# Kernel tuning notes

Hardware: AMD Instinct MI355X
Metric: run time of the kernel (lower is better)

Reference implementation:

```python
import jax, jax.numpy as jnp
import numpy as np

WCD, WCOV, WQUAL = 1.0, 1e-4, 1e-4
BIG = 1e10  # penalty to exclude zero-rows from min/argmin


def _calus(x, y):
    # x: [B, N, 3], y: [B, M, 3]
    B, N, _ = x.shape
    M = y.shape[1]
    # _remove_zero_rows filters rows whose coordinate SUM is zero -> mask instead
    mx = x.sum(-1) != 0  # [B, N] valid x points
    my = y.sum(-1) != 0  # [B, M] valid y points
    dt = x.dtype
    # squared pairwise distances d[b, j, i] = ||x[b,i] - y[b,j]||^2  (expanded form)
    xn = jnp.sum(x * x, axis=-1)  # [B, N]
    yn = jnp.sum(y * y, axis=-1)  # [B, M]
    d = yn[:, :, None] + xn[:, None, :] - 2.0 * jnp.einsum('bmc,bnc->bmn', y, x)  # [B, M, N]
    # push invalid rows/cols out of every min
    d = d + jnp.where(mx, 0.0, BIG).astype(dt)[:, None, :] \
          + jnp.where(my, 0.0, BIG).astype(dt)[:, :, None]
    x_min = jnp.min(d, axis=1)     # [B, N] nearest-y distance per x point
    x_arg = jnp.argmin(d, axis=1)  # [B, N] index into y
    y_min = jnp.min(d, axis=2)     # [B, M] nearest-x distance per y point
    y_arg = jnp.argmin(d, axis=2)  # [B, M] index into x
    fmx, fmy = mx.astype(dt), my.astype(dt)
    nx, ny = fmx.sum(-1), fmy.sum(-1)  # valid counts per sample
    # chamfer = mean over x-points + mean over y-points (torch cat+sum)
    cd = jnp.sum(x_min * fmx, -1) / nx + jnp.sum(y_min * fmy, -1) / ny  # [B]
    # coverage: fraction of y indices hit by some valid x point (unique count)
    rows = jnp.arange(B)[:, None]
    hit_y = jnp.zeros((B, M), dt).at[rows, x_arg].max(fmx)
    cov = hit_y.sum(-1) / ny  # [B]
    # quality: fraction of x indices hit by some valid y point
    hit_x = jnp.zeros((B, N), dt).at[rows, y_arg].max(fmy)
    qual = hit_x.sum(-1) / nx  # [B]
    return cd.mean(), cov.mean(), qual.mean()


def setup_inputs() -> dict:
    key = jax.random.key(0)
    kx, ky = jax.random.split(key)
    B, N, M = 32, 2048, 2048
    x = jax.random.normal(kx, (B, N, 3), dtype=jnp.float32)
    y = jax.random.normal(ky, (B, M, 3), dtype=jnp.float32)
    return {"x": x, "y": y}


def reference(x, y):
    cd, cov, qual = _calus(x, y)
    val = WCD * cd - WCOV * cov - WQUAL * qual
    return (val, cd, cov, qual)
```

## Files before the change

### kernel.cpp

```cpp
#include <hip/hip_runtime.h>
#include <stdint.h>


#define BB 32
#define NP 2048
#define NPTS (BB * NP)
#define BIGF 1e10f

typedef unsigned int u32;

__global__ __launch_bounds__(256) void pack_kernel(const float* __restrict__ x,
                                                   const float* __restrict__ y,
                                                   float4* __restrict__ pk) {
  int t = blockIdx.x * 256 + threadIdx.x;
  int side = t >> 16;
  int i = t & (NPTS - 1);
  const float* src = side ? y : x;
  float v0 = src[3 * i], v1 = src[3 * i + 1], v2 = src[3 * i + 2];
  float vn = v0 * v0 + v1 * v1 + v2 * v2;
  if (v0 + v1 + v2 == 0.0f) vn += BIGF;
  pk[t] = make_float4(v0, v1, v2, vn);
}

#define EMB(d, jg) __uint_as_float((__float_as_uint(d) & 0xFFFFF800u) | (u32)(jg))

__global__ __launch_bounds__(512) void nn_kernel(const float4* __restrict__ pk,
                                                 u32* __restrict__ hitpart,
                                                 float* __restrict__ sums_part,
                                                 float* __restrict__ cnts_part) {
  int bid = blockIdx.x;
  int side = bid >> 8;
  int b = (bid >> 3) & 31;
  int pc = bid & 7;
  int tid = threadIdx.x;
  int w = __builtin_amdgcn_readfirstlane(tid >> 6);
  int lane = tid & 63;

  __shared__ u32 merged[8][256];
  __shared__ float pws[256];
  __shared__ u32 hitlds[64];
  __shared__ float redc[8], redn[8];

  const float4* pbase = pk + side * NPTS + b * NP + pc * 256;
  float pmx[4], pmy[4], pmz[4];
  for (int k = 0; k < 4; ++k) {
    float4 p = pbase[lane + 64 * k];
    pmx[k] = -2.0f * p.x; pmy[k] = -2.0f * p.y; pmz[k] = -2.0f * p.z;
    if (w == 0) pws[lane + 64 * k] = p.w;
  }
  if (tid < 64) hitlds[tid] = 0u;

  const float4* qq = pk + (side ^ 1) * NPTS + b * NP + w * 256;
  u32 qoff = (u32)(w * 256);
  float best0 = 3.0e38f, best1 = 3.0e38f, best2 = 3.0e38f, best3 = 3.0e38f;

#define PROC2(qA, qB, jg)                                                          \
  {                                                                                \
    float a0 = fmaf((qA).x, pmx[0], fmaf((qA).y, pmy[0], fmaf((qA).z, pmz[0], (qA).w))); \
    float a1 = fmaf((qA).x, pmx[1], fmaf((qA).y, pmy[1], fmaf((qA).z, pmz[1], (qA).w))); \
    float a2 = fmaf((qA).x, pmx[2], fmaf((qA).y, pmy[2], fmaf((qA).z, pmz[2], (qA).w))); \
    float a3 = fmaf((qA).x, pmx[3], fmaf((qA).y, pmy[3], fmaf((qA).z, pmz[3], (qA).w))); \
    float b0 = fmaf((qB).x, pmx[0], fmaf((qB).y, pmy[0], fmaf((qB).z, pmz[0], (qB).w))); \
    float b1 = fmaf((qB).x, pmx[1], fmaf((qB).y, pmy[1], fmaf((qB).z, pmz[1], (qB).w))); \
    float b2 = fmaf((qB).x, pmx[2], fmaf((qB).y, pmy[2], fmaf((qB).z, pmz[2], (qB).w))); \
    float b3 = fmaf((qB).x, pmx[3], fmaf((qB).y, pmy[3], fmaf((qB).z, pmz[3], (qB).w))); \
    best0 = fminf(fminf(best0, EMB(a0, jg)), EMB(b0, (jg) + 1));                   \
    best1 = fminf(fminf(best1, EMB(a1, jg)), EMB(b1, (jg) + 1));                   \
    best2 = fminf(fminf(best2, EMB(a2, jg)), EMB(b2, (jg) + 1));                   \
    best3 = fminf(fminf(best3, EMB(a3, jg)), EMB(b3, (jg) + 1));                   \
  }

  float4 qa0 = qq[0], qa1 = qq[1], qa2 = qq[2], qa3 = qq[3];
  for (int jc = 0; jc < 256; jc += 8) {
    float4 qb0 = qq[jc + 4], qb1 = qq[jc + 5], qb2 = qq[jc + 6], qb3 = qq[jc + 7];
    u32 jg = qoff + (u32)jc;
    PROC2(qa0, qa1, jg);
    PROC2(qa2, qa3, jg + 2);
    qa0 = qq[jc + 8]; qa1 = qq[jc + 9]; qa2 = qq[jc + 10]; qa3 = qq[jc + 11];
    PROC2(qb0, qb1, jg + 4);
    PROC2(qb2, qb3, jg + 6);
  }

  merged[w][lane +   0] = __float_as_uint(best0);
  merged[w][lane +  64] = __float_as_uint(best1);
  merged[w][lane + 128] = __float_as_uint(best2);
  merged[w][lane + 192] = __float_as_uint(best3);
  __syncthreads();

  float contrib = 0.f, cnt = 0.f;
  if (tid < 256) {
    float bd = __uint_as_float(merged[0][tid]);
#pragma unroll
    for (int ww = 1; ww < 8; ++ww) bd = fminf(bd, __uint_as_float(merged[ww][tid]));
    u32 bits = __float_as_uint(bd);
    u32 bi = bits & 0x7FFu;
    float dmin = __uint_as_float(bits & 0xFFFFF800u);
    float pwv = pws[tid];
    bool valid = (pwv < 1e9f);
    contrib = valid ? (dmin + pwv) : 0.f;
    cnt = valid ? 1.f : 0.f;
    if (valid) atomicOr(&hitlds[bi >> 5], 1u << (bi & 31));
  }
  for (int o = 32; o > 0; o >>= 1) {
    contrib += __shfl_down(contrib, o, 64);
    cnt += __shfl_down(cnt, o, 64);
  }
  if (lane == 0 && w < 4) { redc[w] = contrib; redn[w] = cnt; }
  __syncthreads();
  if (tid == 0) {
    sums_part[bid] = redc[0] + redc[1] + redc[2] + redc[3];
    cnts_part[bid] = redn[0] + redn[1] + redn[2] + redn[3];
  }
  if (tid < 64) hitpart[bid * 64 + tid] = hitlds[tid];
}

__global__ __launch_bounds__(512) void assemble_kernel(const u32* __restrict__ hitpart,
                                                       const float* __restrict__ sums_part,
                                                       const float* __restrict__ cnts_part,
                                                       float* __restrict__ out) {
  __shared__ float hs[64], ss[64], cs[64];
  int tid = threadIdx.x;
  int sb = tid >> 3, c = tid & 7;
  float h = 0.f;
  for (int wd = c; wd < 64; wd += 8) {
    u32 m = 0u;
#pragma unroll
    for (int blk = 0; blk < 8; ++blk) m |= hitpart[(sb * 8 + blk) * 64 + wd];
    h += (float)__popc(m);
  }
  h += __shfl_down(h, 4, 8);
  h += __shfl_down(h, 2, 8);
  h += __shfl_down(h, 1, 8);
  if (c == 0) {
    float s = 0.f, n = 0.f;
#pragma unroll
    for (int blk = 0; blk < 8; ++blk) {
      s += sums_part[sb * 8 + blk];
      n += cnts_part[sb * 8 + blk];
    }
    hs[sb] = h; ss[sb] = s; cs[sb] = n;
  }
  __syncthreads();
  if (tid < 64) {
    float cd = 0.f, cov = 0.f, qual = 0.f;
    if (tid < BB) {
      float nx = cs[tid], ny = cs[BB + tid];
      cd = ss[tid] / nx + ss[BB + tid] / ny;
      cov = hs[tid] / ny;
      qual = hs[BB + tid] / nx;
    }
    for (int o = 32; o > 0; o >>= 1) {
      cd += __shfl_down(cd, o, 64);
      cov += __shfl_down(cov, o, 64);
      qual += __shfl_down(qual, o, 64);
    }
    if (tid == 0) {
      cd /= (float)BB; cov /= (float)BB; qual /= (float)BB;
      out[0] = cd - 1e-4f * cov - 1e-4f * qual;
      out[1] = cd;
      out[2] = cov;
      out[3] = qual;
    }
  }
}

extern "C" void kernel_launch(void* const* d_in, const int* in_sizes, int n_in,
                              void* d_out, int out_size, void* d_ws, size_t ws_size,
                              hipStream_t stream) {
  const float* x = (const float*)d_in[0];
  const float* y = (const float*)d_in[1];
  float* out = (float*)d_out;
  char* ws = (char*)d_ws;

  u32* hitpart = (u32*)ws;
  float* sums_part = (float*)(ws + 131072);
  float* cnts_part = (float*)(ws + 133120);
  float4* pk = (float4*)(ws + 135168);

  pack_kernel<<<2 * NPTS / 256, 256, 0, stream>>>(x, y, pk);
  nn_kernel<<<2 * BB * 8, 512, 0, stream>>>(pk, hitpart, sums_part, cnts_part);
  assemble_kernel<<<1, 512, 0, stream>>>(hitpart, sums_part, cnts_part, out);
}
```

Measured before the change: 103.4 us.

## Use packed FP32 FMA with SoA point pairs and larger 1024-thread blocks

Repacks points into structure-of-arrays float2 pairs (X, Y, Z, norm) so the distance computation can use v_pk_fma_f32, evaluating two candidate points per instruction. The NN kernel now uses 1024-thread blocks, each owning 512 query points with 8 accumulators per lane, and launches half as many blocks; the assemble kernel is adjusted to the new partial count. The goal is to roughly halve the FMA issue cost of the inner loop. In exchange it raises register pressure, adds more waves to the cross-wave min merge, and lowers the number of blocks available for load balance.

Measured after the change: 95.26 us. -7.9%, faster.

```diff
diff --git a/kernel.cpp b/kernel.cpp
--- a/kernel.cpp
+++ b/kernel.cpp
@@ -4,94 +4,116 @@
 
 #define BB 32
 #define NP 2048
-#define NPTS (BB * NP)
 #define BIGF 1e10f
 
 typedef unsigned int u32;
-
-__global__ __launch_bounds__(256) void pack_kernel(const float* __restrict__ x,
-                                                   const float* __restrict__ y,
-                                                   float4* __restrict__ pk) {
+typedef float f2 __attribute__((ext_vector_type(2)));
+
+#define EMB(d, jg) __uint_as_float((__float_as_uint(d) & 0xFFFFF800u) | (u32)(jg))
+
+__device__ __forceinline__ f2 pk_fma(f2 a, f2 b, f2 c) {
+  f2 d;
+  asm("v_pk_fma_f32 %0, %1, %2, %3" : "=v"(d) : "v"(a), "v"(b), "v"(c));
+  return d;
+}
+
+__global__ __launch_bounds__(256) void pack2_kernel(const float* __restrict__ x,
+                                                    const float* __restrict__ y,
+                                                    f2* __restrict__ qsX, f2* __restrict__ qsY,
+                                                    f2* __restrict__ qsZ, f2* __restrict__ qsW) {
   int t = blockIdx.x * 256 + threadIdx.x;
-  int side = t >> 16;
-  int i = t & (NPTS - 1);
-  const float* src = side ? y : x;
-  float v0 = src[3 * i], v1 = src[3 * i + 1], v2 = src[3 * i + 2];
-  float vn = v0 * v0 + v1 * v1 + v2 * v2;
-  if (v0 + v1 + v2 == 0.0f) vn += BIGF;
-  pk[t] = make_float4(v0, v1, v2, vn);
-}
-
-#define EMB(d, jg) __uint_as_float((__float_as_uint(d) & 0xFFFFF800u) | (u32)(jg))
-
-__global__ __launch_bounds__(512) void nn_kernel(const float4* __restrict__ pk,
-                                                 u32* __restrict__ hitpart,
-                                                 float* __restrict__ sums_part,
-                                                 float* __restrict__ cnts_part) {
+  int side = t >> 15;
+  int i = t & 32767;
+  const float* src = (side ? y : x) + 6 * i;
+  float a0 = src[0], a1 = src[1], a2 = src[2];
+  float b0 = src[3], b1 = src[4], b2 = src[5];
+  float na = a0 * a0 + a1 * a1 + a2 * a2;
+  float nb = b0 * b0 + b1 * b1 + b2 * b2;
+  if (a0 + a1 + a2 == 0.0f) na += BIGF;
+  if (b0 + b1 + b2 == 0.0f) nb += BIGF;
+  qsX[t] = (f2){a0, b0};
+  qsY[t] = (f2){a1, b1};
+  qsZ[t] = (f2){a2, b2};
+  qsW[t] = (f2){na, nb};
+}
+
+__device__ __forceinline__ void procrec(f2 qx2, f2 qy2, f2 qz2, f2 qw2, u32 jg,
+                                        const f2* pmx, const f2* pmy, const f2* pmz,
+                                        float* best) {
+#pragma unroll
+  for (int k = 0; k < 8; ++k) {
+    f2 d2 = pk_fma(qx2, pmx[k], pk_fma(qy2, pmy[k], pk_fma(qz2, pmz[k], qw2)));
+    best[k] = fminf(fminf(best[k], EMB(d2.x, jg)), EMB(d2.y, jg + 1));
+  }
+}
+
+__global__ __launch_bounds__(1024) __attribute__((amdgpu_waves_per_eu(4, 4)))
+void nn_kernel(const f2* __restrict__ qsX, const f2* __restrict__ qsY,
+               const f2* __restrict__ qsZ, const f2* __restrict__ qsW,
+               u32* __restrict__ hitpart, float* __restrict__ sums_part,
+               float* __restrict__ cnts_part) {
   int bid = blockIdx.x;
-  int side = bid >> 8;
-  int b = (bid >> 3) & 31;
-  int pc = bid & 7;
+  int side = bid >> 7;
+  int b = (bid >> 2) & 31;
+  int pc = bid & 3;
   int tid = threadIdx.x;
   int w = __builtin_amdgcn_readfirstlane(tid >> 6);
   int lane = tid & 63;
 
-  __shared__ u32 merged[8][256];
-  __shared__ float pws[256];
+  __shared__ u32 merged[16][512];
+  __shared__ float pws[512];
   __shared__ u32 hitlds[64];
   __shared__ float redc[8], redn[8];
 
-  const float4* pbase = pk + side * NPTS + b * NP + pc * 256;
-  float pmx[4], pmy[4], pmz[4];
+  int prec0 = side * 32768 + b * 1024 + pc * 256;
+  f2 pmx[8], pmy[8], pmz[8];
+  float best[8];
+#pragma unroll
   for (int k = 0; k < 4; ++k) {
-    float4 p = pbase[lane + 64 * k];
-    pmx[k] = -2.0f * p.x; pmy[k] = -2.0f * p.y; pmz[k] = -2.0f * p.z;
-    if (w == 0) pws[lane + 64 * k] = p.w;
-  }
+    int rec = prec0 + lane + 64 * k;
+    f2 px = qsX[rec], py = qsY[rec], pz = qsZ[rec], pw = qsW[rec];
+    pmx[2 * k] = (f2){-2.f * px.x, -2.f * px.x};
+    pmx[2 * k + 1] = (f2){-2.f * px.y, -2.f * px.y};
+    pmy[2 * k] = (f2){-2.f * py.x, -2.f * py.x};
+    pmy[2 * k + 1] = (f2){-2.f * py.y, -2.f * py.y};
+    pmz[2 * k] = (f2){-2.f * pz.x, -2.f * pz.x};
+    pmz[2 * k + 1] = (f2){-2.f * pz.y, -2.f * pz.y};
+    if (w == 0) ((f2*)pws)[lane + 64 * k] = pw;
+  }
+#pragma unroll
+  for (int k = 0; k < 8; ++k) best[k] = 3.0e38f;
   if (tid < 64) hitlds[tid] = 0u;
 
-  const float4* qq = pk + (side ^ 1) * NPTS + b * NP + w * 256;
-  u32 qoff = (u32)(w * 256);
-  float best0 = 3.0e38f, best1 = 3.0e38f, best2 = 3.0e38f, best3 = 3.0e38f;
-
-#define PROC2(qA, qB, jg)                                                          \
-  {                                                                                \
-    float a0 = fmaf((qA).x, pmx[0], fmaf((qA).y, pmy[0], fmaf((qA).z, pmz[0], (qA).w))); \
-    float a1 = fmaf((qA).x, pmx[1], fmaf((qA).y, pmy[1], fmaf((qA).z, pmz[1], (qA).w))); \
-    float a2 = fmaf((qA).x, pmx[2], fmaf((qA).y, pmy[2], fmaf((qA).z, pmz[2], (qA).w))); \
-    float a3 = fmaf((qA).x, pmx[3], fmaf((qA).y, pmy[3], fmaf((qA).z, pmz[3], (qA).w))); \
-    float b0 = fmaf((qB).x, pmx[0], fmaf((qB).y, pmy[0], fmaf((qB).z, pmz[0], (qB).w))); \
-    float b1 = fmaf((qB).x, pmx[1], fmaf((qB).y, pmy[1], fmaf((qB).z, pmz[1], (qB).w))); \
-    float b2 = fmaf((qB).x, pmx[2], fmaf((qB).y, pmy[2], fmaf((qB).z, pmz[2], (qB).w))); \
-    float b3 = fmaf((qB).x, pmx[3], fmaf((qB).y, pmy[3], fmaf((qB).z, pmz[3], (qB).w))); \
-    best0 = fminf(fminf(best0, EMB(a0, jg)), EMB(b0, (jg) + 1));                   \
-    best1 = fminf(fminf(best1, EMB(a1, jg)), EMB(b1, (jg) + 1));                   \
-    best2 = fminf(fminf(best2, EMB(a2, jg)), EMB(b2, (jg) + 1));                   \
-    best3 = fminf(fminf(best3, EMB(a3, jg)), EMB(b3, (jg) + 1));                   \
-  }
-
-  float4 qa0 = qq[0], qa1 = qq[1], qa2 = qq[2], qa3 = qq[3];
-  for (int jc = 0; jc < 256; jc += 8) {
-    float4 qb0 = qq[jc + 4], qb1 = qq[jc + 5], qb2 = qq[jc + 6], qb3 = qq[jc + 7];
-    u32 jg = qoff + (u32)jc;
-    PROC2(qa0, qa1, jg);
-    PROC2(qa2, qa3, jg + 2);
-    qa0 = qq[jc + 8]; qa1 = qq[jc + 9]; qa2 = qq[jc + 10]; qa3 = qq[jc + 11];
-    PROC2(qb0, qb1, jg + 4);
-    PROC2(qb2, qb3, jg + 6);
-  }
-
-  merged[w][lane +   0] = __float_as_uint(best0);
-  merged[w][lane +  64] = __float_as_uint(best1);
-  merged[w][lane + 128] = __float_as_uint(best2);
-  merged[w][lane + 192] = __float_as_uint(best3);
+  int qrec0 = (side ^ 1) * 32768 + b * 1024 + w * 64;
+  const f2* qX = qsX + qrec0;
+  const f2* qY = qsY + qrec0;
+  const f2* qZ = qsZ + qrec0;
+  const f2* qW = qsW + qrec0;
+  u32 j0 = (u32)(w * 128);
+
+  f2 x0 = qX[0], y0 = qY[0], z0 = qZ[0], w0 = qW[0];
+  f2 x1 = qX[1], y1 = qY[1], z1 = qZ[1], w1 = qW[1];
+  for (int r = 0; r < 64; r += 2) {
+    f2 x2 = qX[r + 2], y2 = qY[r + 2], z2 = qZ[r + 2], w2 = qW[r + 2];
+    f2 x3 = qX[r + 3], y3 = qY[r + 3], z3 = qZ[r + 3], w3 = qW[r + 3];
+    procrec(x0, y0, z0, w0, j0 + 2 * r, pmx, pmy, pmz, best);
+    procrec(x1, y1, z1, w1, j0 + 2 * r + 2, pmx, pmy, pmz, best);
+    x0 = x2; y0 = y2; z0 = z2; w0 = w2;
+    x1 = x3; y1 = y3; z1 = z3; w1 = w3;
+  }
+
+#pragma unroll
+  for (int k = 0; k < 4; ++k) {
+    uint2 v = make_uint2(__float_as_uint(best[2 * k]), __float_as_uint(best[2 * k + 1]));
+    *(uint2*)&merged[w][2 * (lane + 64 * k)] = v;
+  }
   __syncthreads();
 
   float contrib = 0.f, cnt = 0.f;
-  if (tid < 256) {
+  if (tid < 512) {
     float bd = __uint_as_float(merged[0][tid]);
 #pragma unroll
-    for (int ww = 1; ww < 8; ++ww) bd = fminf(bd, __uint_as_float(merged[ww][tid]));
+    for (int ww = 1; ww < 16; ++ww) bd = fminf(bd, __uint_as_float(merged[ww][tid]));
     u32 bits = __float_as_uint(bd);
     u32 bi = bits & 0x7FFu;
     float dmin = __uint_as_float(bits & 0xFFFFF800u);
@@ -105,11 +127,14 @@
     contrib += __shfl_down(contrib, o, 64);
     cnt += __shfl_down(cnt, o, 64);
   }
-  if (lane == 0 && w < 4) { redc[w] = contrib; redn[w] = cnt; }
+  if (tid < 512 && lane == 0) { redc[tid >> 6] = contrib; redn[tid >> 6] = cnt; }
   __syncthreads();
   if (tid == 0) {
-    sums_part[bid] = redc[0] + redc[1] + redc[2] + redc[3];
-    cnts_part[bid] = redn[0] + redn[1] + redn[2] + redn[3];
+    float s = 0.f, n = 0.f;
+#pragma unroll
+    for (int i = 0; i < 8; ++i) { s += redc[i]; n += redn[i]; }
+    sums_part[bid] = s;
+    cnts_part[bid] = n;
   }
   if (tid < 64) hitpart[bid * 64 + tid] = hitlds[tid];
 }
@@ -125,7 +150,7 @@
   for (int wd = c; wd < 64; wd += 8) {
     u32 m = 0u;
 #pragma unroll
-    for (int blk = 0; blk < 8; ++blk) m |= hitpart[(sb * 8 + blk) * 64 + wd];
+    for (int blk = 0; blk < 4; ++blk) m |= hitpart[(sb * 4 + blk) * 64 + wd];
     h += (float)__popc(m);
   }
   h += __shfl_down(h, 4, 8);
@@ -134,9 +159,9 @@
   if (c == 0) {
     float s = 0.f, n = 0.f;
 #pragma unroll
-    for (int blk = 0; blk < 8; ++blk) {
-      s += sums_part[sb * 8 + blk];
-      n += cnts_part[sb * 8 + blk];
+    for (int blk = 0; blk < 4; ++blk) {
+      s += sums_part[sb * 4 + blk];
+      n += cnts_part[sb * 4 + blk];
     }
     hs[sb] = h; ss[sb] = s; cs[sb] = n;
   }
@@ -172,12 +197,16 @@
   float* out = (float*)d_out;
   char* ws = (char*)d_ws;
 
+  const size_t QSZ = (65536 + 8) * sizeof(f2);
   u32* hitpart = (u32*)ws;
-  float* sums_part = (float*)(ws + 131072);
-  float* cnts_part = (float*)(ws + 133120);
-  float4* pk = (float4*)(ws + 135168);
-
-  pack_kernel<<<2 * NPTS / 256, 256, 0, stream>>>(x, y, pk);
-  nn_kernel<<<2 * BB * 8, 512, 0, stream>>>(pk, hitpart, sums_part, cnts_part);
+  float* sums_part = (float*)(ws + 65536);
+  float* cnts_part = (float*)(ws + 66560);
+  f2* qsX = (f2*)(ws + 67584);
+  f2* qsY = (f2*)(ws + 67584 + QSZ);
+  f2* qsZ = (f2*)(ws + 67584 + 2 * QSZ);
+  f2* qsW = (f2*)(ws + 67584 + 3 * QSZ);
+
+  pack2_kernel<<<256, 256, 0, stream>>>(x, y, qsX, qsY, qsZ, qsW);
+  nn_kernel<<<256, 1024, 0, stream>>>(qsX, qsY, qsZ, qsW, hitpart, sums_part, cnts_part);
   assemble_kernel<<<1, 512, 0, stream>>>(hitpart, sums_part, cnts_part, out);
 }
```

## Fuse point packing into NN kernel with LDS staging and packed-FP32 math

Applied to the files above, without the earlier changes.

Removes the separate pack kernel. Each block now loads the raw xyz of the opposite cloud, computes norms and the zero-row penalty, and stages the points in shared memory in an interleaved pair layout. The inner distance loop then uses 2-wide float vectors so the compiler can emit packed FMA instructions, and occupancy is pinned with waves_per_eu. This saves one launch and the global round trip of the packed buffer. In exchange every block recomputes the packing for 2048 points, and 32KB of LDS per block may limit occupancy.

Result: faster. 92.77 us (-10.3%).

```diff
diff --git a/kernel.cpp b/kernel.cpp
--- a/kernel.cpp
+++ b/kernel.cpp
@@ -4,30 +4,18 @@
 
 #define BB 32
 #define NP 2048
-#define NPTS (BB * NP)
 #define BIGF 1e10f
 
 typedef unsigned int u32;
-
-__global__ __launch_bounds__(256) void pack_kernel(const float* __restrict__ x,
-                                                   const float* __restrict__ y,
-                                                   float4* __restrict__ pk) {
-  int t = blockIdx.x * 256 + threadIdx.x;
-  int side = t >> 16;
-  int i = t & (NPTS - 1);
-  const float* src = side ? y : x;
-  float v0 = src[3 * i], v1 = src[3 * i + 1], v2 = src[3 * i + 2];
-  float vn = v0 * v0 + v1 * v1 + v2 * v2;
-  if (v0 + v1 + v2 == 0.0f) vn += BIGF;
-  pk[t] = make_float4(v0, v1, v2, vn);
-}
+typedef float f2 __attribute__((ext_vector_type(2)));
 
 #define EMB(d, jg) __uint_as_float((__float_as_uint(d) & 0xFFFFF800u) | (u32)(jg))
 
-__global__ __launch_bounds__(512) void nn_kernel(const float4* __restrict__ pk,
-                                                 u32* __restrict__ hitpart,
-                                                 float* __restrict__ sums_part,
-                                                 float* __restrict__ cnts_part) {
+__global__ __launch_bounds__(512) __attribute__((amdgpu_waves_per_eu(4, 4)))
+void nn_fused_kernel(const float* __restrict__ x, const float* __restrict__ y,
+                     u32* __restrict__ hitpart, float* __restrict__ sums_part,
+                     float* __restrict__ cnts_part) {
+#pragma clang fp contract(fast)
   int bid = blockIdx.x;
   int side = bid >> 8;
   int b = (bid >> 3) & 31;
@@ -36,55 +24,73 @@
   int w = __builtin_amdgcn_readfirstlane(tid >> 6);
   int lane = tid & 63;
 
+  __shared__ float4 qs[2048];
   __shared__ u32 merged[8][256];
   __shared__ float pws[256];
   __shared__ u32 hitlds[64];
-  __shared__ float redc[8], redn[8];
+  __shared__ float redc[4], redn[4];
 
-  const float4* pbase = pk + side * NPTS + b * NP + pc * 256;
-  float pmx[4], pmy[4], pmz[4];
+  {
+    const float* qraw = (side ? x : y) + b * NP * 3 + tid * 12;
+    float4 f0 = *(const float4*)(qraw);
+    float4 f1 = *(const float4*)(qraw + 4);
+    float4 g2 = *(const float4*)(qraw + 8);
+    float n0 = f0.x * f0.x + f0.y * f0.y + f0.z * f0.z;
+    float n1 = f0.w * f0.w + f1.x * f1.x + f1.y * f1.y;
+    float n2 = f1.z * f1.z + f1.w * f1.w + g2.x * g2.x;
+    float n3 = g2.y * g2.y + g2.z * g2.z + g2.w * g2.w;
+    if (f0.x + f0.y + f0.z == 0.f) n0 += BIGF;
+    if (f0.w + f1.x + f1.y == 0.f) n1 += BIGF;
+    if (f1.z + f1.w + g2.x == 0.f) n2 += BIGF;
+    if (g2.y + g2.z + g2.w == 0.f) n3 += BIGF;
+    qs[4 * tid + 0] = make_float4(f0.x, f0.w, f0.y, f1.x);
+    qs[4 * tid + 1] = make_float4(f0.z, f1.y, n0, n1);
+    qs[4 * tid + 2] = make_float4(f1.z, g2.y, f1.w, g2.z);
+    qs[4 * tid + 3] = make_float4(g2.x, g2.w, n2, n3);
+  }
+
+  const float* praw = (side ? y : x) + (b * NP + pc * 256) * 3;
+  f2 pmx[4], pmy[4], pmz[4];
+  float best[4];
+#pragma unroll
   for (int k = 0; k < 4; ++k) {
-    float4 p = pbase[lane + 64 * k];
-    pmx[k] = -2.0f * p.x; pmy[k] = -2.0f * p.y; pmz[k] = -2.0f * p.z;
-    if (w == 0) pws[lane + 64 * k] = p.w;
+    int pl = lane + 64 * k;
+    float p0 = praw[3 * pl], p1 = praw[3 * pl + 1], p2 = praw[3 * pl + 2];
+    pmx[k] = (f2){-2.f * p0, -2.f * p0};
+    pmy[k] = (f2){-2.f * p1, -2.f * p1};
+    pmz[k] = (f2){-2.f * p2, -2.f * p2};
+    if (w == 0) {
+      float pn = p0 * p0 + p1 * p1 + p2 * p2;
+      if (p0 + p1 + p2 == 0.f) pn += BIGF;
+      pws[pl] = pn;
+    }
+    best[k] = 3.0e38f;
   }
   if (tid < 64) hitlds[tid] = 0u;
+  __syncthreads();
 
-  const float4* qq = pk + (side ^ 1) * NPTS + b * NP + w * 256;
-  u32 qoff = (u32)(w * 256);
-  float best0 = 3.0e38f, best1 = 3.0e38f, best2 = 3.0e38f, best3 = 3.0e38f;
-
-#define PROC2(qA, qB, jg)                                                          \
-  {                                                                                \
-    float a0 = fmaf((qA).x, pmx[0], fmaf((qA).y, pmy[0], fmaf((qA).z, pmz[0], (qA).w))); \
-    float a1 = fmaf((qA).x, pmx[1], fmaf((qA).y, pmy[1], fmaf((qA).z, pmz[1], (qA).w))); \
-    float a2 = fmaf((qA).x, pmx[2], fmaf((qA).y, pmy[2], fmaf((qA).z, pmz[2], (qA).w))); \
-    float a3 = fmaf((qA).x, pmx[3], fmaf((qA).y, pmy[3], fmaf((qA).z, pmz[3], (qA).w))); \
-    float b0 = fmaf((qB).x, pmx[0], fmaf((qB).y, pmy[0], fmaf((qB).z, pmz[0], (qB).w))); \
-    float b1 = fmaf((qB).x, pmx[1], fmaf((qB).y, pmy[1], fmaf((qB).z, pmz[1], (qB).w))); \
-    float b2 = fmaf((qB).x, pmx[2], fmaf((qB).y, pmy[2], fmaf((qB).z, pmz[2], (qB).w))); \
-    float b3 = fmaf((qB).x, pmx[3], fmaf((qB).y, pmy[3], fmaf((qB).z, pmz[3], (qB).w))); \
-    best0 = fminf(fminf(best0, EMB(a0, jg)), EMB(b0, (jg) + 1));                   \
-    best1 = fminf(fminf(best1, EMB(a1, jg)), EMB(b1, (jg) + 1));                   \
-    best2 = fminf(fminf(best2, EMB(a2, jg)), EMB(b2, (jg) + 1));                   \
-    best3 = fminf(fminf(best3, EMB(a3, jg)), EMB(b3, (jg) + 1));                   \
+  const float4* qr = &qs[w * 256];
+  u32 j0 = (u32)(w * 256);
+#pragma unroll 4
+  for (int r = 0; r < 128; ++r) {
+    float4 A = qr[2 * r];
+    float4 B = qr[2 * r + 1];
+    f2 qx2 = (f2){A.x, A.y};
+    f2 qy2 = (f2){A.z, A.w};
+    f2 qz2 = (f2){B.x, B.y};
+    f2 qw2 = (f2){B.z, B.w};
+    u32 jg = j0 + 2 * (u32)r;
+#pragma unroll
+    for (int k = 0; k < 4; ++k) {
+      f2 d2 = qx2 * pmx[k] + (qy2 * pmy[k] + (qz2 * pmz[k] + qw2));
+      best[k] = fminf(fminf(best[k], EMB(d2.x, jg)), EMB(d2.y, jg + 1));
+    }
   }
 
-  float4 qa0 = qq[0], qa1 = qq[1], qa2 = qq[2], qa3 = qq[3];
-  for (int jc = 0; jc < 256; jc += 8) {
-    float4 qb0 = qq[jc + 4], qb1 = qq[jc + 5], qb2 = qq[jc + 6], qb3 = qq[jc + 7];
-    u32 jg = qoff + (u32)jc;
-    PROC2(qa0, qa1, jg);
-    PROC2(qa2, qa3, jg + 2);
-    qa0 = qq[jc + 8]; qa1 = qq[jc + 9]; qa2 = qq[jc + 10]; qa3 = qq[jc + 11];
-    PROC2(qb0, qb1, jg + 4);
-    PROC2(qb2, qb3, jg + 6);
-  }
-
-  merged[w][lane +   0] = __float_as_uint(best0);
-  merged[w][lane +  64] = __float_as_uint(best1);
-  merged[w][lane + 128] = __float_as_uint(best2);
-  merged[w][lane + 192] = __float_as_uint(best3);
+  merged[w][lane +   0] = __float_as_uint(best[0]);
+  merged[w][lane +  64] = __float_as_uint(best[1]);
+  merged[w][lane + 128] = __float_as_uint(best[2]);
+  merged[w][lane + 192] = __float_as_uint(best[3]);
   __syncthreads();
 
   float contrib = 0.f, cnt = 0.f;
@@ -105,7 +111,7 @@
     contrib += __shfl_down(contrib, o, 64);
     cnt += __shfl_down(cnt, o, 64);
   }
-  if (lane == 0 && w < 4) { redc[w] = contrib; redn[w] = cnt; }
+  if (tid < 256 && lane == 0) { redc[w] = contrib; redn[w] = cnt; }
   __syncthreads();
   if (tid == 0) {
     sums_part[bid] = redc[0] + redc[1] + redc[2] + redc[3];
@@ -175,9 +181,7 @@
   u32* hitpart = (u32*)ws;
   float* sums_part = (float*)(ws + 131072);
   float* cnts_part = (float*)(ws + 133120);
-  float4* pk = (float4*)(ws + 135168);
 
-  pack_kernel<<<2 * NPTS / 256, 256, 0, stream>>>(x, y, pk);
-  nn_kernel<<<2 * BB * 8, 512, 0, stream>>>(pk, hitpart, sums_part, cnts_part);
+  nn_fused_kernel<<<512, 512, 0, stream>>>(x, y, hitpart, sums_part, cnts_part);
   assemble_kernel<<<1, 512, 0, stream>>>(hitpart, sums_part, cnts_part, out);
 }
```

## Compute pairwise distances with bf16 MFMA using split-precision operand packing

Applied to the files above, without the earlier changes.

Replaces the scalar FMA distance loop with 16x16x32 bf16 MFMA instructions. Each coordinate and norm is split into hi/lo bf16 parts and packed into K=32 rows, so the dot product reconstructs near-fp32 squared distances including both norms. The packed operands are written by the pack kernel, and the per-point validity check now reads the raw input again. This trades extra pack-kernel traffic (64B per point per operand) and a residual precision error for matrix-core throughput on the N×M distance computation.

Measured after the change: 109.8 us. +6.2%, slower.

```diff
diff --git a/kernel.cpp b/kernel.cpp
--- a/kernel.cpp
+++ b/kernel.cpp
@@ -4,30 +4,66 @@
 
 #define BB 32
 #define NP 2048
-#define NPTS (BB * NP)
 #define BIGF 1e10f
 
 typedef unsigned int u32;
+typedef unsigned short u16;
+typedef __bf16 bf16x8 __attribute__((ext_vector_type(8)));
+typedef float f32x4 __attribute__((ext_vector_type(4)));
+
+__device__ __forceinline__ u16 bf16rne(float f) {
+  u32 u = __float_as_uint(f);
+  return (u16)((u + 0x7FFFu + ((u >> 16) & 1u)) >> 16);
+}
+__device__ __forceinline__ float bf2f(u16 h) { return __uint_as_float((u32)h << 16); }
+__device__ __forceinline__ u32 pk2(u16 a, u16 b) { return (u32)a | ((u32)b << 16); }
 
 __global__ __launch_bounds__(256) void pack_kernel(const float* __restrict__ x,
                                                    const float* __restrict__ y,
-                                                   float4* __restrict__ pk) {
+                                                   u16* __restrict__ ap,
+                                                   u16* __restrict__ bp) {
   int t = blockIdx.x * 256 + threadIdx.x;
-  int side = t >> 16;
-  int i = t & (NPTS - 1);
-  const float* src = side ? y : x;
-  float v0 = src[3 * i], v1 = src[3 * i + 1], v2 = src[3 * i + 2];
-  float vn = v0 * v0 + v1 * v1 + v2 * v2;
-  if (v0 + v1 + v2 == 0.0f) vn += BIGF;
-  pk[t] = make_float4(v0, v1, v2, vn);
-}
-
-#define EMB(d, jg) __uint_as_float((__float_as_uint(d) & 0xFFFFF800u) | (u32)(jg))
-
-__global__ __launch_bounds__(512) void nn_kernel(const float4* __restrict__ pk,
-                                                 u32* __restrict__ hitpart,
-                                                 float* __restrict__ sums_part,
-                                                 float* __restrict__ cnts_part) {
+  int cloud = t >> 16;
+  int g = t & 65535;
+  const float* src = (cloud ? y : x) + 3 * g;
+  float v[3] = {src[0], src[1], src[2]};
+  float n = v[0] * v[0] + v[1] * v[1] + v[2] * v[2];
+  if (v[0] + v[1] + v[2] == 0.0f) n += BIGF;
+
+  u16 h[3], l[3], mh[3], ml[3];
+#pragma unroll
+  for (int i = 0; i < 3; ++i) {
+    h[i] = bf16rne(v[i]);
+    l[i] = bf16rne(v[i] - bf2f(h[i]));
+    float m = -2.0f * v[i];
+    mh[i] = bf16rne(m);
+    ml[i] = bf16rne(m - bf2f(mh[i]));
+  }
+  u16 nh = bf16rne(n);
+  float r1 = n - bf2f(nh);
+  u16 nm = bf16rne(r1);
+  u16 nl = bf16rne(r1 - bf2f(nm));
+  const u16 ONE = 0x3F80;
+
+  uint4* a4 = (uint4*)(ap + (size_t)t * 32);
+  uint4* b4 = (uint4*)(bp + (size_t)t * 32);
+  a4[0] = make_uint4(pk2(h[0], h[1]), pk2(h[2], l[0]), pk2(l[1], l[2]), pk2(h[0], h[1]));
+  a4[1] = make_uint4(pk2(h[2], nh), pk2(nm, nl), pk2(ONE, ONE), pk2(ONE, 0));
+  a4[2] = make_uint4(0, 0, 0, 0);
+  a4[3] = make_uint4(0, 0, 0, 0);
+  b4[0] = make_uint4(pk2(mh[0], mh[1]), pk2(mh[2], mh[0]), pk2(mh[1], mh[2]), pk2(ml[0], ml[1]));
+  b4[1] = make_uint4(pk2(ml[2], ONE), pk2(ONE, ONE), pk2(nh, nm), pk2(nl, 0));
+  b4[2] = make_uint4(0, 0, 0, 0);
+  b4[3] = make_uint4(0, 0, 0, 0);
+}
+
+__global__ __launch_bounds__(512, 4) void nn_kernel(const u16* __restrict__ ap,
+                                                    const u16* __restrict__ bp,
+                                                    const float* __restrict__ x,
+                                                    const float* __restrict__ y,
+                                                    u32* __restrict__ hitpart,
+                                                    float* __restrict__ sums_part,
+                                                    float* __restrict__ cnts_part) {
   int bid = blockIdx.x;
   int side = bid >> 8;
   int b = (bid >> 3) & 31;
@@ -35,56 +71,57 @@
   int tid = threadIdx.x;
   int w = __builtin_amdgcn_readfirstlane(tid >> 6);
   int lane = tid & 63;
+  int quad = lane >> 4, m16 = lane & 15;
 
   __shared__ u32 merged[8][256];
-  __shared__ float pws[256];
   __shared__ u32 hitlds[64];
-  __shared__ float redc[8], redn[8];
-
-  const float4* pbase = pk + side * NPTS + b * NP + pc * 256;
-  float pmx[4], pmy[4], pmz[4];
-  for (int k = 0; k < 4; ++k) {
-    float4 p = pbase[lane + 64 * k];
-    pmx[k] = -2.0f * p.x; pmy[k] = -2.0f * p.y; pmz[k] = -2.0f * p.z;
-    if (w == 0) pws[lane + 64 * k] = p.w;
-  }
+  __shared__ float redc[4], redn[4];
+
+  int cloudA = side ^ 1;
+  int cloudB = side;
+  const uint4* a4 = (const uint4*)ap;
+  const uint4* b4 = (const uint4*)bp;
+
+  bf16x8 Bf[16];
+#pragma unroll
+  for (int pt = 0; pt < 16; ++pt) {
+    int rowB = cloudB * 65536 + b * 2048 + pc * 256 + pt * 16 + m16;
+    Bf[pt] = __builtin_bit_cast(bf16x8, b4[rowB * 4 + quad]);
+  }
+  float best[16];
+#pragma unroll
+  for (int pt = 0; pt < 16; ++pt) best[pt] = 3.0e38f;
   if (tid < 64) hitlds[tid] = 0u;
 
-  const float4* qq = pk + (side ^ 1) * NPTS + b * NP + w * 256;
-  u32 qoff = (u32)(w * 256);
-  float best0 = 3.0e38f, best1 = 3.0e38f, best2 = 3.0e38f, best3 = 3.0e38f;
-
-#define PROC2(qA, qB, jg)                                                          \
-  {                                                                                \
-    float a0 = fmaf((qA).x, pmx[0], fmaf((qA).y, pmy[0], fmaf((qA).z, pmz[0], (qA).w))); \
-    float a1 = fmaf((qA).x, pmx[1], fmaf((qA).y, pmy[1], fmaf((qA).z, pmz[1], (qA).w))); \
-    float a2 = fmaf((qA).x, pmx[2], fmaf((qA).y, pmy[2], fmaf((qA).z, pmz[2], (qA).w))); \
-    float a3 = fmaf((qA).x, pmx[3], fmaf((qA).y, pmy[3], fmaf((qA).z, pmz[3], (qA).w))); \
-    float b0 = fmaf((qB).x, pmx[0], fmaf((qB).y, pmy[0], fmaf((qB).z, pmz[0], (qB).w))); \
-    float b1 = fmaf((qB).x, pmx[1], fmaf((qB).y, pmy[1], fmaf((qB).z, pmz[1], (qB).w))); \
-    float b2 = fmaf((qB).x, pmx[2], fmaf((qB).y, pmy[2], fmaf((qB).z, pmz[2], (qB).w))); \
-    float b3 = fmaf((qB).x, pmx[3], fmaf((qB).y, pmy[3], fmaf((qB).z, pmz[3], (qB).w))); \
-    best0 = fminf(fminf(best0, EMB(a0, jg)), EMB(b0, (jg) + 1));                   \
-    best1 = fminf(fminf(best1, EMB(a1, jg)), EMB(b1, (jg) + 1));                   \
-    best2 = fminf(fminf(best2, EMB(a2, jg)), EMB(b2, (jg) + 1));                   \
-    best3 = fminf(fminf(best3, EMB(a3, jg)), EMB(b3, (jg) + 1));                   \
-  }
-
-  float4 qa0 = qq[0], qa1 = qq[1], qa2 = qq[2], qa3 = qq[3];
-  for (int jc = 0; jc < 256; jc += 8) {
-    float4 qb0 = qq[jc + 4], qb1 = qq[jc + 5], qb2 = qq[jc + 6], qb3 = qq[jc + 7];
-    u32 jg = qoff + (u32)jc;
-    PROC2(qa0, qa1, jg);
-    PROC2(qa2, qa3, jg + 2);
-    qa0 = qq[jc + 8]; qa1 = qq[jc + 9]; qa2 = qq[jc + 10]; qa3 = qq[jc + 11];
-    PROC2(qb0, qb1, jg + 4);
-    PROC2(qb2, qb3, jg + 6);
-  }
-
-  merged[w][lane +   0] = __float_as_uint(best0);
-  merged[w][lane +  64] = __float_as_uint(best1);
-  merged[w][lane + 128] = __float_as_uint(best2);
-  merged[w][lane + 192] = __float_as_uint(best3);
+  int rowA0 = cloudA * 65536 + b * 2048 + w * 256 + m16;
+  u32 jq = (u32)(quad * 4);
+  f32x4 zc = {0.f, 0.f, 0.f, 0.f};
+  uint4 araw = a4[rowA0 * 4 + quad];
+  for (int qt = 0; qt < 16; ++qt) {
+    uint4 anext = a4[(rowA0 + ((qt + 1) & 15) * 16) * 4 + quad];
+    bf16x8 Af = __builtin_bit_cast(bf16x8, araw);
+    u32 jtq = (u32)(w * 256 + qt * 16) + jq;
+#pragma unroll
+    for (int pt = 0; pt < 16; ++pt) {
+      f32x4 d = __builtin_amdgcn_mfma_f32_16x16x32_bf16(Af, Bf[pt], zc, 0, 0, 0);
+      u32 e0 = (__float_as_uint(d[0]) & 0xFFFFF800u) | jtq;
+      u32 e1 = (__float_as_uint(d[1]) & 0xFFFFF800u) | (jtq + 1);
+      u32 e2 = (__float_as_uint(d[2]) & 0xFFFFF800u) | (jtq + 2);
+      u32 e3 = (__float_as_uint(d[3]) & 0xFFFFF800u) | (jtq + 3);
+      float m01 = fminf(__uint_as_float(e0), __uint_as_float(e1));
+      float m23 = fminf(__uint_as_float(e2), __uint_as_float(e3));
+      best[pt] = fminf(best[pt], fminf(m01, m23));
+    }
+    araw = anext;
+  }
+
+#pragma unroll
+  for (int pt = 0; pt < 16; ++pt) {
+    float v = best[pt];
+    v = fminf(v, __shfl_xor(v, 16, 64));
+    v = fminf(v, __shfl_xor(v, 32, 64));
+    if (lane < 16) merged[w][pt * 16 + lane] = __float_as_uint(v);
+  }
   __syncthreads();
 
   float contrib = 0.f, cnt = 0.f;
@@ -95,9 +132,10 @@
     u32 bits = __float_as_uint(bd);
     u32 bi = bits & 0x7FFu;
     float dmin = __uint_as_float(bits & 0xFFFFF800u);
-    float pwv = pws[tid];
-    bool valid = (pwv < 1e9f);
-    contrib = valid ? (dmin + pwv) : 0.f;
+    const float* praw = (side ? y : x) + (b * NP + pc * 256 + tid) * 3;
+    float p0 = praw[0], p1 = praw[1], p2 = praw[2];
+    bool valid = (p0 + p1 + p2) != 0.f;
+    contrib = valid ? dmin : 0.f;
     cnt = valid ? 1.f : 0.f;
     if (valid) atomicOr(&hitlds[bi >> 5], 1u << (bi & 31));
   }
@@ -105,7 +143,7 @@
     contrib += __shfl_down(contrib, o, 64);
     cnt += __shfl_down(cnt, o, 64);
   }
-  if (lane == 0 && w < 4) { redc[w] = contrib; redn[w] = cnt; }
+  if (tid < 256 && lane == 0) { redc[tid >> 6] = contrib; redn[tid >> 6] = cnt; }
   __syncthreads();
   if (tid == 0) {
     sums_part[bid] = redc[0] + redc[1] + redc[2] + redc[3];
@@ -175,9 +213,10 @@
   u32* hitpart = (u32*)ws;
   float* sums_part = (float*)(ws + 131072);
   float* cnts_part = (float*)(ws + 133120);
-  float4* pk = (float4*)(ws + 135168);
-
-  pack_kernel<<<2 * NPTS / 256, 256, 0, stream>>>(x, y, pk);
-  nn_kernel<<<2 * BB * 8, 512, 0, stream>>>(pk, hitpart, sums_part, cnts_part);
+  u16* ap = (u16*)(ws + 135168);
+  u16* bp = (u16*)(ws + 135168 + 8388608ull);
+
+  pack_kernel<<<512, 256, 0, stream>>>(x, y, ap, bp);
+  nn_kernel<<<512, 512, 0, stream>>>(ap, bp, x, y, hitpart, sums_part, cnts_part);
   assemble_kernel<<<1, 512, 0, stream>>>(hitpart, sums_part, cnts_part, out);
 }
```
